# Kernel tuning notes

Hardware: AMD Instinct MI355X
Metric: run time of the kernel (lower is better)

Reference implementation:

```python
import jax, jax.numpy as jnp
import numpy as np

B, S, V, E, H, T = 512, 512, 5000, 100, 128, 25
HD = H // 2          # per-direction LSTM hidden size
START, STOP = 1, 2   # tag_map['START'], tag_map['STOP']


def setup_inputs() -> dict:
    key = jax.random.key(0)
    ks = jax.random.split(key, 20)
    sc = 0.1
    transitions = jax.random.normal(ks[0], (T, T), dtype=jnp.float32)
    transitions = transitions.at[:, START].set(-1000.0)
    transitions = transitions.at[STOP, :].set(-1000.0)
    return {
        "sentences": jax.random.randint(ks[1], (B, S), 0, V),
        "tags": jax.random.randint(ks[2], (B, S), 0, T),
        "embed": jax.random.normal(ks[3], (V, E), dtype=jnp.float32) * sc,
        # torch nn.LSTM weights, gate order (i, f, g, o), forward + backward dirs
        "W_ih_f": jax.random.normal(ks[4], (4 * HD, E), dtype=jnp.float32) * sc,
        "W_hh_f": jax.random.normal(ks[5], (4 * HD, HD), dtype=jnp.float32) * sc,
        "b_ih_f": jax.random.normal(ks[6], (4 * HD,), dtype=jnp.float32) * sc,
        "b_hh_f": jax.random.normal(ks[7], (4 * HD,), dtype=jnp.float32) * sc,
        "W_ih_b": jax.random.normal(ks[8], (4 * HD, E), dtype=jnp.float32) * sc,
        "W_hh_b": jax.random.normal(ks[9], (4 * HD, HD), dtype=jnp.float32) * sc,
        "b_ih_b": jax.random.normal(ks[10], (4 * HD,), dtype=jnp.float32) * sc,
        "b_hh_b": jax.random.normal(ks[11], (4 * HD,), dtype=jnp.float32) * sc,
        # init_hidden() uses randn initial states; materialized here as inputs
        "h0": jax.random.normal(ks[12], (2, B, HD), dtype=jnp.float32),
        "c0": jax.random.normal(ks[13], (2, B, HD), dtype=jnp.float32),
        "W_out": jax.random.normal(ks[14], (T, H), dtype=jnp.float32) * sc,
        "b_out": jax.random.normal(ks[15], (T,), dtype=jnp.float32) * sc,
        "transitions": transitions,
    }


def _lstm_dir(x, Wih, Whh, bih, bhh, h0, c0, reverse):
    # x: [B, S, E] -> outputs [B, S, HD]; torch gate order i, f, g, o
    def step(carry, xt):
        h, c = carry
        z = xt @ Wih.T + h @ Whh.T + (bih + bhh)  # [B, 4*HD]
        i, f, g, o = jnp.split(z, 4, axis=-1)
        c = jax.nn.sigmoid(f) * c + jax.nn.sigmoid(i) * jnp.tanh(g)
        h = jax.nn.sigmoid(o) * jnp.tanh(c)
        return (h, c), h
    _, hs = jax.lax.scan(step, (h0, c0), jnp.swapaxes(x, 0, 1), reverse=reverse)
    return jnp.swapaxes(hs, 0, 1)


def reference(sentences, tags, embed, W_ih_f, W_hh_f, b_ih_f, b_hh_f,
              W_ih_b, W_hh_b, b_ih_b, b_hh_b, h0, c0, W_out, b_out, transitions):
    # ---- BiLSTM features (eval mode: single-layer LSTM, dropout inactive) ----
    emb = embed[sentences]  # [B, S, E]
    hf = _lstm_dir(emb, W_ih_f, W_hh_f, b_ih_f, b_hh_f, h0[0], c0[0], False)
    hb = _lstm_dir(emb, W_ih_b, W_hh_b, b_ih_b, b_hh_b, h0[1], c0[1], True)
    logits = jnp.concatenate([hf, hb], axis=-1) @ W_out.T + b_out  # [B, S, T]

    # ---- real_path_score (gold path), batched ----
    lab = jnp.concatenate(
        [jnp.full((B, 1), START, dtype=tags.dtype), tags], axis=1)  # [B, S+1]
    em = jnp.take_along_axis(logits, lab[:, 1:, None], axis=2)[..., 0].sum(-1)
    tr = transitions[lab[:, :-1], lab[:, 1:]].sum(-1) + transitions[lab[:, -1], STOP]
    real = em + tr  # [B]

    # ---- total_score: CRF forward algorithm (previous starts at zeros, as in source) ----
    def fstep(prev, lt):  # prev [B, T], lt [B, T]
        # scores[b, i, j] = prev[b, i] + trans[i, j] + lt[b, j]
        sc = prev[:, :, None] + transitions[None, :, :] + lt[:, None, :]
        return jax.nn.logsumexp(sc, axis=1), None
    prev, _ = jax.lax.scan(fstep, jnp.zeros((B, T), logits.dtype),
                           jnp.swapaxes(logits, 0, 1))
    total = jax.nn.logsumexp(prev + transitions[:, STOP][None, :], axis=1)  # [B]

    # neg_log_likelihood sums over the batch
    return jnp.sum(total - real)
```

## Files before the change

kernel.cpp:

```cpp
#include <hip/hip_runtime.h>
#include <hip/hip_bf16.h>
#include <cstdint>

#define B_ 512
#define S_ 512
#define V_ 5000
#define E_ 100
#define HD_ 64
#define T_ 25
#define START_ 1
#define STOP_ 2

typedef _Float16 half2_t __attribute__((ext_vector_type(2)));
typedef __attribute__((ext_vector_type(8))) short short8;
typedef __attribute__((ext_vector_type(4))) float f32x4;

#if __has_builtin(__builtin_amdgcn_fdot2)
__device__ inline float dot2(uint32_t a, uint32_t b, float c) {
  return __builtin_amdgcn_fdot2(__builtin_bit_cast(half2_t, a),
                                __builtin_bit_cast(half2_t, b), c, false);
}
#else
__device__ inline float dot2(uint32_t a, uint32_t b, float c) {
  half2_t ha = __builtin_bit_cast(half2_t, a);
  half2_t hb = __builtin_bit_cast(half2_t, b);
  return c + (float)ha[0] * (float)hb[0] + (float)ha[1] * (float)hb[1];
}
#endif

__device__ inline float sigm(float x) { return 1.0f / (1.0f + __expf(-x)); }
__device__ inline float tanh_(float x) { return 1.0f - 2.0f / (1.0f + __expf(2.0f * x)); }

__global__ __launch_bounds__(256) void k_proj(const float* __restrict__ embed,
                                              const float* __restrict__ Wf,
                                              const float* __restrict__ Wb,
                                              float* __restrict__ Pf,
                                              float* __restrict__ Pb) {
  __shared__ __align__(16) float embS[16 * E_];
  int v0 = blockIdx.x * 16;
  const float* Wih = blockIdx.y ? Wb : Wf;
  float* P = blockIdx.y ? Pb : Pf;
  int nv = V_ - v0; if (nv > 16) nv = 16;
  for (int idx = threadIdx.x; idx < nv * E_; idx += 256)
    embS[idx] = embed[v0 * E_ + idx];
  __syncthreads();
  int u = threadIdx.x;
  float acc[16];
#pragma unroll
  for (int i = 0; i < 16; i++) acc[i] = 0.f;
  const float4* W4 = (const float4*)(Wih + u * E_);
  const float4* e4 = (const float4*)embS;
#pragma unroll 5
  for (int q = 0; q < 25; q++) {
    float4 w = W4[q];
#pragma unroll
    for (int vi = 0; vi < 16; vi++) {
      float4 e = e4[vi * 25 + q];
      acc[vi] += w.x * e.x + w.y * e.y + w.z * e.z + w.w * e.w;
    }
  }
  int pk = (u & 63) * 4 + (u >> 6);
  for (int vi = 0; vi < nv; vi++)
    P[(size_t)(v0 + vi) * 256 + pk] = acc[vi];
}

__global__ __launch_bounds__(256) void k_prep(const float* __restrict__ Wout,
                                              __hip_bfloat16* __restrict__ WoutP) {
  int idx = blockIdx.x * 256 + threadIdx.x;
  if (idx < 32 * 128) {
    int r = idx >> 7, c = idx & 127;
    float v = (r < T_) ? Wout[r * 128 + c] : 0.f;
    WoutP[idx] = __float2bfloat16(v);
  }
}

__global__ __attribute__((amdgpu_waves_per_eu(1, 1))) __launch_bounds__(64)
void k_lstm(
    const int* __restrict__ sentences,
    const float* __restrict__ Pf, const float* __restrict__ Pb,
    const float* __restrict__ Whh_f, const float* __restrict__ Whh_b,
    const float* __restrict__ bih_f, const float* __restrict__ bhh_f,
    const float* __restrict__ bih_b, const float* __restrict__ bhh_b,
    const float* __restrict__ h0, const float* __restrict__ c0,
    __hip_bfloat16* __restrict__ feat) {
  int j = threadIdx.x;
  int seq = blockIdx.x;
  int be = seq & (B_ - 1);
  int d = seq >> 9;
  const float* P   = d ? Pb : Pf;
  const float* Whh = d ? Whh_b : Whh_f;
  const float* bih = d ? bih_b : bih_f;
  const float* bhh = d ? bhh_b : bhh_f;

  __shared__ __align__(16) uint32_t hS[32];

  uint32_t wp[4][32];
  float bg[4];
#pragma unroll
  for (int g = 0; g < 4; g++) {
    int u = g * 64 + j;
    const float4* rp = (const float4*)(Whh + (size_t)u * HD_);
#pragma unroll
    for (int q = 0; q < 16; q++) {
      float4 a = rp[q];
      union { _Float16 h[2]; uint32_t u32; } p0, p1;
      p0.h[0] = (_Float16)a.x; p0.h[1] = (_Float16)a.y;
      p1.h[0] = (_Float16)a.z; p1.h[1] = (_Float16)a.w;
      wp[g][2 * q] = p0.u32; wp[g][2 * q + 1] = p1.u32;
    }
    bg[g] = bih[u] + bhh[u];
  }
  float c = c0[(d * B_ + be) * HD_ + j];
  ((_Float16*)hS)[j] = (_Float16)h0[(d * B_ + be) * HD_ + j];
  asm volatile("s_waitcnt lgkmcnt(0)" ::: "memory");

  const int* sent = sentences + (size_t)be * S_;
  int tt0 = d ? (S_ - 1) : 0;
  int stp = d ? -1 : 1;
  int tok1 = sent[tt0];
  const float4* P4 = (const float4*)P;
  float4 x = P4[(size_t)tok1 * 64 + j];
  tok1 = sent[tt0 + stp];
  const uint4* hS4 = (const uint4*)hS;

  for (int t = 0; t < S_; t++) {
    int tt = tt0 + stp * t;
    float4 xn = x;
    if (t + 1 < S_) xn = P4[(size_t)tok1 * 64 + j];
    int tok2 = tok1;
    if (t + 2 < S_) tok2 = sent[tt + 2 * stp];

    float ac[4][4];
#pragma unroll
    for (int g = 0; g < 4; g++)
#pragma unroll
      for (int i = 0; i < 4; i++) ac[g][i] = 0.f;
#pragma unroll
    for (int q = 0; q < 8; q++) {
      uint4 hv = hS4[q];
      int kp = 4 * q;
#pragma unroll
      for (int g = 0; g < 4; g++) {
        ac[g][0] = dot2(wp[g][kp + 0], hv.x, ac[g][0]);
        ac[g][1] = dot2(wp[g][kp + 1], hv.y, ac[g][1]);
        ac[g][2] = dot2(wp[g][kp + 2], hv.z, ac[g][2]);
        ac[g][3] = dot2(wp[g][kp + 3], hv.w, ac[g][3]);
      }
    }
    float zi = (ac[0][0] + ac[0][1]) + (ac[0][2] + ac[0][3]) + bg[0] + x.x;
    float zf = (ac[1][0] + ac[1][1]) + (ac[1][2] + ac[1][3]) + bg[1] + x.y;
    float zg = (ac[2][0] + ac[2][1]) + (ac[2][2] + ac[2][3]) + bg[2] + x.z;
    float zo = (ac[3][0] + ac[3][1]) + (ac[3][2] + ac[3][3]) + bg[3] + x.w;
    c = sigm(zf) * c + sigm(zi) * tanh_(zg);
    float hh = sigm(zo) * tanh_(c);
    feat[((size_t)be * S_ + tt) * 128 + d * 64 + j] = __float2bfloat16(hh);
    ((_Float16*)hS)[j] = (_Float16)hh;
    asm volatile("s_waitcnt lgkmcnt(0)" ::: "memory");
    x = xn;
    tok1 = tok2;
  }
}

__global__ __launch_bounds__(256) void k_logits(const __hip_bfloat16* __restrict__ feat,
                                                const __hip_bfloat16* __restrict__ WoutP,
                                                const float* __restrict__ bout,
                                                float* __restrict__ logits) {
  int w = threadIdx.x >> 6, l = threadIdx.x & 63;
  size_t r0 = ((size_t)blockIdx.x * 4 + w) * 16;
  int mrow = l & 15, kg = l >> 4;
  short8 bfr[2][4];
#pragma unroll
  for (int nt = 0; nt < 2; nt++) {
    int n = nt * 16 + mrow;
#pragma unroll
    for (int kb = 0; kb < 4; kb++)
      bfr[nt][kb] = *(const short8*)(WoutP + n * 128 + kb * 32 + kg * 8);
  }
  f32x4 acc[2];
#pragma unroll
  for (int nt = 0; nt < 2; nt++) {
    int col = nt * 16 + mrow;
    float bb = (col < T_) ? bout[col] : 0.f;
    acc[nt] = (f32x4){bb, bb, bb, bb};
  }
#pragma unroll
  for (int kb = 0; kb < 4; kb++) {
    short8 a = *(const short8*)(feat + (r0 + mrow) * 128 + kb * 32 + kg * 8);
    acc[0] = __builtin_amdgcn_mfma_f32_16x16x32_bf16(a, bfr[0][kb], acc[0], 0, 0, 0);
    acc[1] = __builtin_amdgcn_mfma_f32_16x16x32_bf16(a, bfr[1][kb], acc[1], 0, 0, 0);
  }
#pragma unroll
  for (int nt = 0; nt < 2; nt++) {
    int col = nt * 16 + mrow;
    if (col < T_) {
#pragma unroll
      for (int q = 0; q < 4; q++) {
        int row = kg * 4 + q;
        logits[(r0 + row) * T_ + col] = acc[nt][q];
      }
    }
  }
}

__global__ __launch_bounds__(64) void k_crf(const float* __restrict__ logits,
                                            const float* __restrict__ trans,
                                            float* __restrict__ totals) {
  int j = threadIdx.x;
  int b = blockIdx.x;
  bool act = j < T_;
  __shared__ __align__(16) float qS[32];
  float Ecol[T_];
#pragma unroll
  for (int i = 0; i < T_; i++)
    Ecol[i] = act ? __expf(trans[i * T_ + j]) : 0.f;
  if (j >= T_ && j < 32) qS[j] = 0.f;
  float tstop = act ? trans[j * T_ + STOP_] : 0.f;
  float prev = act ? 0.f : -INFINITY;
  const float* lg = logits + (size_t)b * S_ * T_;
  float ltn = act ? lg[j] : 0.f;
  asm volatile("s_waitcnt lgkmcnt(0)" ::: "memory");
  for (int t = 0; t < S_; t++) {
    float lt = ltn;
    if (t + 1 < S_) ltn = act ? lg[(size_t)(t + 1) * T_ + j] : 0.f;
    float m = __builtin_bit_cast(float,
        __builtin_amdgcn_readfirstlane(__builtin_bit_cast(int, prev)));
    float q = __expf(prev - m);
    if (act) qS[j] = q;
    asm volatile("s_waitcnt lgkmcnt(0)" ::: "memory");
    const float4* q4 = (const float4*)qS;
    float4 qv0 = q4[0], qv1 = q4[1], qv2 = q4[2], qv3 = q4[3];
    float4 qv4 = q4[4], qv5 = q4[5], qv6 = q4[6];
    float s0, s1, s2, s3;
    s0 = qv0.x * Ecol[0];  s1 = qv0.y * Ecol[1];
    s2 = qv0.z * Ecol[2];  s3 = qv0.w * Ecol[3];
    s0 += qv1.x * Ecol[4];  s1 += qv1.y * Ecol[5];
    s2 += qv1.z * Ecol[6];  s3 += qv1.w * Ecol[7];
    s0 += qv2.x * Ecol[8];  s1 += qv2.y * Ecol[9];
    s2 += qv2.z * Ecol[10]; s3 += qv2.w * Ecol[11];
    s0 += qv3.x * Ecol[12]; s1 += qv3.y * Ecol[13];
    s2 += qv3.z * Ecol[14]; s3 += qv3.w * Ecol[15];
    s0 += qv4.x * Ecol[16]; s1 += qv4.y * Ecol[17];
    s2 += qv4.z * Ecol[18]; s3 += qv4.w * Ecol[19];
    s0 += qv5.x * Ecol[20]; s1 += qv5.y * Ecol[21];
    s2 += qv5.z * Ecol[22]; s3 += qv5.w * Ecol[23];
    s0 += qv6.x * Ecol[24];
    float s = (s0 + s1) + (s2 + s3);
    prev = lt + m + __logf(s);
    if (!act) prev = -INFINITY;
  }
  float v = prev + tstop;
  float m = v;
#pragma unroll
  for (int off = 32; off > 0; off >>= 1)
    m = fmaxf(m, __shfl_xor(m, off, 64));
  float e = __expf(v - m);
#pragma unroll
  for (int off = 32; off > 0; off >>= 1)
    e += __shfl_xor(e, off, 64);
  if (j == 0) totals[b] = m + __logf(e);
}

__global__ __launch_bounds__(256) void k_real(const float* __restrict__ logits,
                                              const int* __restrict__ tags,
                                              const float* __restrict__ trans,
                                              float* __restrict__ reals) {
  __shared__ float red[256];
  int b = blockIdx.x;
  float acc = 0.f;
  for (int s = threadIdx.x; s < S_; s += 256) {
    int tg = tags[(size_t)b * S_ + s];
    int pv = (s == 0) ? START_ : tags[(size_t)b * S_ + s - 1];
    acc += logits[((size_t)b * S_ + s) * T_ + tg] + trans[pv * T_ + tg];
  }
  red[threadIdx.x] = acc;
  __syncthreads();
  for (int off = 128; off > 0; off >>= 1) {
    if (threadIdx.x < off) red[threadIdx.x] += red[threadIdx.x + off];
    __syncthreads();
  }
  if (threadIdx.x == 0)
    reals[b] = red[0] + trans[tags[(size_t)b * S_ + S_ - 1] * T_ + STOP_];
}

__global__ __launch_bounds__(256) void k_final(const float* __restrict__ totals,
                                               const float* __restrict__ reals,
                                               float* __restrict__ out) {
  __shared__ float red[256];
  float acc = 0.f;
  for (int b = threadIdx.x; b < B_; b += 256) acc += totals[b] - reals[b];
  red[threadIdx.x] = acc;
  __syncthreads();
  for (int off = 128; off > 0; off >>= 1) {
    if (threadIdx.x < off) red[threadIdx.x] += red[threadIdx.x + off];
    __syncthreads();
  }
  if (threadIdx.x == 0) out[0] = red[0];
}

extern "C" void kernel_launch(void* const* d_in, const int* in_sizes, int n_in,
                              void* d_out, int out_size, void* d_ws, size_t ws_size,
                              hipStream_t stream) {
  const int*   sentences = (const int*)d_in[0];
  const int*   tags  = (const int*)d_in[1];
  const float* embed = (const float*)d_in[2];
  const float* Wih_f = (const float*)d_in[3];
  const float* Whh_f = (const float*)d_in[4];
  const float* bih_f = (const float*)d_in[5];
  const float* bhh_f = (const float*)d_in[6];
  const float* Wih_b = (const float*)d_in[7];
  const float* Whh_b = (const float*)d_in[8];
  const float* bih_b = (const float*)d_in[9];
  const float* bhh_b = (const float*)d_in[10];
  const float* h0    = (const float*)d_in[11];
  const float* c0    = (const float*)d_in[12];
  const float* Wout  = (const float*)d_in[13];
  const float* bout  = (const float*)d_in[14];
  const float* trans = (const float*)d_in[15];

  char* ws = (char*)d_ws;
  float* Pf = (float*)(ws);
  float* Pb = (float*)(ws + 5120000);
  __hip_bfloat16* feat = (__hip_bfloat16*)(ws + 10240000);
  float* logits = (float*)(ws + 10240000 + 67108864);
  __hip_bfloat16* WoutP = (__hip_bfloat16*)(ws + 10240000 + 67108864 + 26214400);
  float* totals = (float*)(ws + 10240000 + 67108864 + 26214400 + 8192);
  float* reals  = totals + B_;
  float* out    = (float*)d_out;

  k_proj<<<dim3(313, 2), 256, 0, stream>>>(embed, Wih_f, Wih_b, Pf, Pb);
  k_prep<<<16, 256, 0, stream>>>(Wout, WoutP);
  k_lstm<<<1024, 64, 0, stream>>>(sentences, Pf, Pb, Whh_f, Whh_b,
                                  bih_f, bhh_f, bih_b, bhh_b, h0, c0, feat);
  k_logits<<<4096, 256, 0, stream>>>(feat, WoutP, bout, logits);
  k_crf<<<512, 64, 0, stream>>>(logits, trans, totals);
  k_real<<<512, 256, 0, stream>>>(logits, tags, trans, reals);
  k_final<<<1, 256, 0, stream>>>(totals, reals, out);
}
```

Baseline: 557.3 us.

## Batch LSTM recurrence over 16 sequences per block using fp16 MFMA

Replaces the one-sequence-per-wave dot2 LSTM with blocks that each handle 16 sequences, computing the combined [h, x] times [Whh; Wih] gate matmul with 16x16x32 f16 MFMA. The precomputed token projection table is dropped: embeddings are converted to padded fp16 and the input projection is fused into the per-step matmul. Only 64 blocks run, so parallelism falls sharply and each step pays a __syncthreads, though per-step work is far more efficient. The input projection now runs in fp16 rather than fp32, which may slightly change accuracy.

```diff
diff --git a/kernel.cpp b/kernel.cpp
--- a/kernel.cpp
+++ b/kernel.cpp
@@ -11,61 +11,44 @@
 #define START_ 1
 #define STOP_ 2
 
-typedef _Float16 half2_t __attribute__((ext_vector_type(2)));
 typedef __attribute__((ext_vector_type(8))) short short8;
 typedef __attribute__((ext_vector_type(4))) float f32x4;
-
-#if __has_builtin(__builtin_amdgcn_fdot2)
-__device__ inline float dot2(uint32_t a, uint32_t b, float c) {
-  return __builtin_amdgcn_fdot2(__builtin_bit_cast(half2_t, a),
-                                __builtin_bit_cast(half2_t, b), c, false);
-}
-#else
-__device__ inline float dot2(uint32_t a, uint32_t b, float c) {
-  half2_t ha = __builtin_bit_cast(half2_t, a);
-  half2_t hb = __builtin_bit_cast(half2_t, b);
-  return c + (float)ha[0] * (float)hb[0] + (float)ha[1] * (float)hb[1];
-}
-#endif
+typedef __attribute__((ext_vector_type(8))) _Float16 f16x8;
 
 __device__ inline float sigm(float x) { return 1.0f / (1.0f + __expf(-x)); }
 __device__ inline float tanh_(float x) { return 1.0f - 2.0f / (1.0f + __expf(2.0f * x)); }
 
-__global__ __launch_bounds__(256) void k_proj(const float* __restrict__ embed,
-                                              const float* __restrict__ Wf,
-                                              const float* __restrict__ Wb,
-                                              float* __restrict__ Pf,
-                                              float* __restrict__ Pb) {
-  __shared__ __align__(16) float embS[16 * E_];
-  int v0 = blockIdx.x * 16;
-  const float* Wih = blockIdx.y ? Wb : Wf;
-  float* P = blockIdx.y ? Pb : Pf;
-  int nv = V_ - v0; if (nv > 16) nv = 16;
-  for (int idx = threadIdx.x; idx < nv * E_; idx += 256)
-    embS[idx] = embed[v0 * E_ + idx];
-  __syncthreads();
-  int u = threadIdx.x;
-  float acc[16];
-#pragma unroll
-  for (int i = 0; i < 16; i++) acc[i] = 0.f;
-  const float4* W4 = (const float4*)(Wih + u * E_);
-  const float4* e4 = (const float4*)embS;
-#pragma unroll 5
-  for (int q = 0; q < 25; q++) {
-    float4 w = W4[q];
-#pragma unroll
-    for (int vi = 0; vi < 16; vi++) {
-      float4 e = e4[vi * 25 + q];
-      acc[vi] += w.x * e.x + w.y * e.y + w.z * e.z + w.w * e.w;
-    }
-  }
-  int pk = (u & 63) * 4 + (u >> 6);
-  for (int vi = 0; vi < nv; vi++)
-    P[(size_t)(v0 + vi) * 256 + pk] = acc[vi];
-}
-
-__global__ __launch_bounds__(256) void k_prep(const float* __restrict__ Wout,
-                                              __hip_bfloat16* __restrict__ WoutP) {
+__device__ inline f32x4 mm16(f16x8 a, f16x8 b, f32x4 c) {
+  return __builtin_amdgcn_mfma_f32_16x16x32_f16(a, b, c, 0, 0, 0);
+}
+
+__global__ __launch_bounds__(256) void k_prep_w(const float* __restrict__ Whh_f,
+                                                const float* __restrict__ Wih_f,
+                                                const float* __restrict__ Whh_b,
+                                                const float* __restrict__ Wih_b,
+                                                _Float16* __restrict__ Wcomb) {
+  int idx = blockIdx.x * 256 + threadIdx.x;
+  if (idx >= 2 * 256 * 192) return;
+  int d = idx / (256 * 192);
+  int rem = idx % (256 * 192);
+  int u = rem / 192, k = rem % 192;
+  const float* Whh = d ? Whh_b : Whh_f;
+  const float* Wih = d ? Wih_b : Wih_f;
+  float v = (k < HD_) ? Whh[u * HD_ + k]
+                      : ((k < HD_ + E_) ? Wih[u * E_ + (k - HD_)] : 0.f);
+  Wcomb[idx] = (_Float16)v;
+}
+
+__global__ __launch_bounds__(256) void k_prep_e(const float* __restrict__ embed,
+                                                _Float16* __restrict__ embP) {
+  int idx = blockIdx.x * 256 + threadIdx.x;
+  if (idx >= V_ * 112) return;
+  int v = idx / 112, e = idx % 112;
+  embP[idx] = (e < E_) ? (_Float16)embed[v * E_ + e] : (_Float16)0.f;
+}
+
+__global__ __launch_bounds__(256) void k_prep_o(const float* __restrict__ Wout,
+                                                __hip_bfloat16* __restrict__ WoutP) {
   int idx = blockIdx.x * 256 + threadIdx.x;
   if (idx < 32 * 128) {
     int r = idx >> 7, c = idx & 127;
@@ -74,90 +57,108 @@
   }
 }
 
-__global__ __attribute__((amdgpu_waves_per_eu(1, 1))) __launch_bounds__(64)
-void k_lstm(
+__global__ __launch_bounds__(256, 1) void k_lstm(
     const int* __restrict__ sentences,
-    const float* __restrict__ Pf, const float* __restrict__ Pb,
-    const float* __restrict__ Whh_f, const float* __restrict__ Whh_b,
+    const _Float16* __restrict__ embP,
+    const _Float16* __restrict__ Wcomb,
     const float* __restrict__ bih_f, const float* __restrict__ bhh_f,
     const float* __restrict__ bih_b, const float* __restrict__ bhh_b,
     const float* __restrict__ h0, const float* __restrict__ c0,
     __hip_bfloat16* __restrict__ feat) {
-  int j = threadIdx.x;
-  int seq = blockIdx.x;
-  int be = seq & (B_ - 1);
-  int d = seq >> 9;
-  const float* P   = d ? Pb : Pf;
-  const float* Whh = d ? Whh_b : Whh_f;
+  int tid = threadIdx.x;
+  int w = tid >> 6, l = tid & 63;
+  int row = tid >> 4, tr = tid & 15;
+  int grp = blockIdx.x & 31, d = blockIdx.x >> 5;
+  int sbase = grp * 16;
   const float* bih = d ? bih_b : bih_f;
   const float* bhh = d ? bhh_b : bhh_f;
 
-  __shared__ __align__(16) uint32_t hS[32];
-
-  uint32_t wp[4][32];
+  __shared__ __align__(16) _Float16 Hs[2][16][72];
+  __shared__ __align__(16) _Float16 Ae[2][16][136];
+
+  int mrow = l & 15, kg = l >> 4;
+  int ucol = w * 16 + mrow;
+  int r0 = kg * 4;
+
+  f16x8 Bf[4][6];
+  const _Float16* Wd = Wcomb + (size_t)d * 256 * 192;
+#pragma unroll
+  for (int g = 0; g < 4; g++) {
+    const _Float16* rp = Wd + (size_t)(g * 64 + ucol) * 192;
+#pragma unroll
+    for (int kt = 0; kt < 6; kt++)
+      Bf[g][kt] = *(const f16x8*)(rp + kt * 32 + kg * 8);
+  }
   float bg[4];
 #pragma unroll
   for (int g = 0; g < 4; g++) {
-    int u = g * 64 + j;
-    const float4* rp = (const float4*)(Whh + (size_t)u * HD_);
-#pragma unroll
-    for (int q = 0; q < 16; q++) {
-      float4 a = rp[q];
-      union { _Float16 h[2]; uint32_t u32; } p0, p1;
-      p0.h[0] = (_Float16)a.x; p0.h[1] = (_Float16)a.y;
-      p1.h[0] = (_Float16)a.z; p1.h[1] = (_Float16)a.w;
-      wp[g][2 * q] = p0.u32; wp[g][2 * q + 1] = p1.u32;
+    int u = g * 64 + ucol;
+    bg[g] = bih[u] + bhh[u];
+  }
+  float cc[4];
+#pragma unroll
+  for (int q = 0; q < 4; q++)
+    cc[q] = c0[(size_t)(d * B_ + sbase + r0 + q) * HD_ + ucol];
+
+  for (int idx = tid; idx < 16 * HD_; idx += 256)
+    Hs[0][idx >> 6][idx & 63] =
+        (_Float16)h0[(size_t)(d * B_ + sbase + (idx >> 6)) * HD_ + (idx & 63)];
+  for (int idx = tid; idx < 2 * 16 * 24; idx += 256) {
+    int bsel = idx / (16 * 24);
+    int rem = idx % (16 * 24);
+    Ae[bsel][rem / 24][112 + rem % 24] = (_Float16)0.f;
+  }
+
+  const int* sent_row = sentences + (size_t)(sbase + row) * S_;
+  int tt0 = d ? (S_ - 1) : 0, stp = d ? -1 : 1;
+  int tok0 = sent_row[tt0];
+  if (tr < 14) {
+    uint4 g0 = ((const uint4*)embP)[(size_t)tok0 * 14 + tr];
+    *(uint4*)(&Ae[0][row][tr * 8]) = g0;
+  }
+  int tokN = sent_row[tt0 + stp];
+  __syncthreads();
+
+  for (int t = 0; t < S_; ++t) {
+    int cur = t & 1, nxt = cur ^ 1;
+    int tt = tt0 + stp * t;
+    uint4 gv;
+    bool havegv = (t + 1 < S_) && (tr < 14);
+    if (havegv) gv = ((const uint4*)embP)[(size_t)tokN * 14 + tr];
+    int tokN2 = tokN;
+    if (t + 2 < S_) tokN2 = sent_row[tt + 2 * stp];
+
+    f16x8 Ah0 = *(const f16x8*)(&Hs[cur][mrow][kg * 8]);
+    f16x8 Ah1 = *(const f16x8*)(&Hs[cur][mrow][32 + kg * 8]);
+    f16x8 Ae0 = *(const f16x8*)(&Ae[cur][mrow][kg * 8]);
+    f16x8 Ae1 = *(const f16x8*)(&Ae[cur][mrow][32 + kg * 8]);
+    f16x8 Ae2 = *(const f16x8*)(&Ae[cur][mrow][64 + kg * 8]);
+    f16x8 Ae3 = *(const f16x8*)(&Ae[cur][mrow][96 + kg * 8]);
+
+    f32x4 acc[4];
+#pragma unroll
+    for (int g = 0; g < 4; g++) {
+      acc[g] = (f32x4){bg[g], bg[g], bg[g], bg[g]};
+      acc[g] = mm16(Ah0, Bf[g][0], acc[g]);
+      acc[g] = mm16(Ah1, Bf[g][1], acc[g]);
+      acc[g] = mm16(Ae0, Bf[g][2], acc[g]);
+      acc[g] = mm16(Ae1, Bf[g][3], acc[g]);
+      acc[g] = mm16(Ae2, Bf[g][4], acc[g]);
+      acc[g] = mm16(Ae3, Bf[g][5], acc[g]);
     }
-    bg[g] = bih[u] + bhh[u];
-  }
-  float c = c0[(d * B_ + be) * HD_ + j];
-  ((_Float16*)hS)[j] = (_Float16)h0[(d * B_ + be) * HD_ + j];
-  asm volatile("s_waitcnt lgkmcnt(0)" ::: "memory");
-
-  const int* sent = sentences + (size_t)be * S_;
-  int tt0 = d ? (S_ - 1) : 0;
-  int stp = d ? -1 : 1;
-  int tok1 = sent[tt0];
-  const float4* P4 = (const float4*)P;
-  float4 x = P4[(size_t)tok1 * 64 + j];
-  tok1 = sent[tt0 + stp];
-  const uint4* hS4 = (const uint4*)hS;
-
-  for (int t = 0; t < S_; t++) {
-    int tt = tt0 + stp * t;
-    float4 xn = x;
-    if (t + 1 < S_) xn = P4[(size_t)tok1 * 64 + j];
-    int tok2 = tok1;
-    if (t + 2 < S_) tok2 = sent[tt + 2 * stp];
-
-    float ac[4][4];
-#pragma unroll
-    for (int g = 0; g < 4; g++)
-#pragma unroll
-      for (int i = 0; i < 4; i++) ac[g][i] = 0.f;
-#pragma unroll
-    for (int q = 0; q < 8; q++) {
-      uint4 hv = hS4[q];
-      int kp = 4 * q;
-#pragma unroll
-      for (int g = 0; g < 4; g++) {
-        ac[g][0] = dot2(wp[g][kp + 0], hv.x, ac[g][0]);
-        ac[g][1] = dot2(wp[g][kp + 1], hv.y, ac[g][1]);
-        ac[g][2] = dot2(wp[g][kp + 2], hv.z, ac[g][2]);
-        ac[g][3] = dot2(wp[g][kp + 3], hv.w, ac[g][3]);
-      }
+#pragma unroll
+    for (int q = 0; q < 4; q++) {
+      float zi = acc[0][q], zf = acc[1][q], zg = acc[2][q], zo = acc[3][q];
+      float c2 = sigm(zf) * cc[q] + sigm(zi) * tanh_(zg);
+      cc[q] = c2;
+      float hh = sigm(zo) * tanh_(c2);
+      Hs[nxt][r0 + q][ucol] = (_Float16)hh;
+      feat[(((size_t)(sbase + r0 + q)) * S_ + tt) * 128 + d * 64 + ucol] =
+          __float2bfloat16(hh);
     }
-    float zi = (ac[0][0] + ac[0][1]) + (ac[0][2] + ac[0][3]) + bg[0] + x.x;
-    float zf = (ac[1][0] + ac[1][1]) + (ac[1][2] + ac[1][3]) + bg[1] + x.y;
-    float zg = (ac[2][0] + ac[2][1]) + (ac[2][2] + ac[2][3]) + bg[2] + x.z;
-    float zo = (ac[3][0] + ac[3][1]) + (ac[3][2] + ac[3][3]) + bg[3] + x.w;
-    c = sigm(zf) * c + sigm(zi) * tanh_(zg);
-    float hh = sigm(zo) * tanh_(c);
-    feat[((size_t)be * S_ + tt) * 128 + d * 64 + j] = __float2bfloat16(hh);
-    ((_Float16*)hS)[j] = (_Float16)hh;
-    asm volatile("s_waitcnt lgkmcnt(0)" ::: "memory");
-    x = xn;
-    tok1 = tok2;
+    if (havegv) *(uint4*)(&Ae[nxt][row][tr * 8]) = gv;
+    tokN = tokN2;
+    __syncthreads();
   }
 }
 
@@ -195,8 +196,8 @@
     if (col < T_) {
 #pragma unroll
       for (int q = 0; q < 4; q++) {
-        int row = kg * 4 + q;
-        logits[(r0 + row) * T_ + col] = acc[nt][q];
+        int rowq = kg * 4 + q;
+        logits[(r0 + rowq) * T_ + col] = acc[nt][q];
       }
     }
   }
@@ -318,19 +319,20 @@
   const float* trans = (const float*)d_in[15];
 
   char* ws = (char*)d_ws;
-  float* Pf = (float*)(ws);
-  float* Pb = (float*)(ws + 5120000);
-  __hip_bfloat16* feat = (__hip_bfloat16*)(ws + 10240000);
-  float* logits = (float*)(ws + 10240000 + 67108864);
-  __hip_bfloat16* WoutP = (__hip_bfloat16*)(ws + 10240000 + 67108864 + 26214400);
-  float* totals = (float*)(ws + 10240000 + 67108864 + 26214400 + 8192);
-  float* reals  = totals + B_;
-  float* out    = (float*)d_out;
-
-  k_proj<<<dim3(313, 2), 256, 0, stream>>>(embed, Wih_f, Wih_b, Pf, Pb);
-  k_prep<<<16, 256, 0, stream>>>(Wout, WoutP);
-  k_lstm<<<1024, 64, 0, stream>>>(sentences, Pf, Pb, Whh_f, Whh_b,
-                                  bih_f, bhh_f, bih_b, bhh_b, h0, c0, feat);
+  __hip_bfloat16* feat  = (__hip_bfloat16*)(ws);
+  float* logits         = (float*)(ws + 67108864);
+  __hip_bfloat16* WoutP = (__hip_bfloat16*)(ws + 67108864 + 26214400);
+  _Float16* Wcomb       = (_Float16*)(ws + 67108864 + 26214400 + 8192);
+  _Float16* embP        = (_Float16*)(ws + 67108864 + 26214400 + 8192 + 196608);
+  float* totals         = (float*)(ws + 67108864 + 26214400 + 8192 + 196608 + 1120000);
+  float* reals          = totals + B_;
+  float* out            = (float*)d_out;
+
+  k_prep_w<<<384, 256, 0, stream>>>(Whh_f, Wih_f, Whh_b, Wih_b, Wcomb);
+  k_prep_e<<<2188, 256, 0, stream>>>(embed, embP);
+  k_prep_o<<<16, 256, 0, stream>>>(Wout, WoutP);
+  k_lstm<<<64, 256, 0, stream>>>(sentences, embP, Wcomb,
+                                 bih_f, bhh_f, bih_b, bhh_b, h0, c0, feat);
   k_logits<<<4096, 256, 0, stream>>>(feat, WoutP, bout, logits);
   k_crf<<<512, 64, 0, stream>>>(logits, trans, totals);
   k_real<<<512, 256, 0, stream>>>(logits, tags, trans, reals);
```

Result: slower. 834.2 us (+49.7%).
